# Optimization experiments

Hardware: AMD Instinct MI355X
Metric: run time of the kernel (lower is better)

Reference implementation:

```python
import jax, jax.numpy as jnp
import numpy as np

D_CONV = 4
D_STATE = 16
DT_RANK = 64


def _silu(x):
    return x * jax.nn.sigmoid(x)


def setup_inputs() -> dict:
    key = jax.random.key(0)
    ks = jax.random.split(key, 10)
    B, L, dim = 2, 1024, 1024
    d_inner = 2 * dim
    s = lambda fan: 1.0 / np.sqrt(fan)
    inp = {
        "x": jax.random.normal(ks[0], (B, L, dim), jnp.float32),
        "ln_w": jnp.ones((dim,), jnp.float32),
        "ln_b": jnp.zeros((dim,), jnp.float32),
        "w_in": jax.random.normal(ks[1], (2 * d_inner, dim), jnp.float32) * s(dim),
        "conv_w": jax.random.normal(ks[2], (d_inner, D_CONV), jnp.float32) * s(D_CONV),
        "conv_b": jnp.zeros((d_inner,), jnp.float32),
        "w_xproj": jax.random.normal(ks[3], (DT_RANK + 2 * D_STATE, d_inner), jnp.float32) * s(d_inner),
        "w_dt": jax.random.normal(ks[4], (d_inner, DT_RANK), jnp.float32) * s(DT_RANK),
        "b_dt": jax.random.normal(ks[5], (d_inner,), jnp.float32) * 0.1,
        # S4D-real init: A = -(1..d_state) per channel
        "a_log": jnp.tile(jnp.log(jnp.arange(1, D_STATE + 1, dtype=jnp.float32)), (d_inner, 1)),
        "d_skip": jnp.ones((d_inner,), jnp.float32),
        "w_out": jax.random.normal(ks[6], (dim, d_inner), jnp.float32) * s(d_inner),
    }
    return inp


def reference(x, ln_w, ln_b, w_in, conv_w, conv_b, w_xproj, w_dt, b_dt, a_log, d_skip, w_out):
    B, L, dim = x.shape
    residual = x

    # LayerNorm
    mu = jnp.mean(x, axis=-1, keepdims=True)
    var = jnp.mean((x - mu) ** 2, axis=-1, keepdims=True)
    xn = (x - mu) * jax.lax.rsqrt(var + 1e-5) * ln_w + ln_b

    # in_proj -> (x_ssm, z) each (B, L, d_inner)
    xz = jnp.einsum("bld,ed->ble", xn, w_in)
    d_inner = xz.shape[-1] // 2
    xs, z = xz[..., :d_inner], xz[..., d_inner:]

    # depthwise causal conv1d (kernel D_CONV) + SiLU
    xp = jnp.pad(xs, ((0, 0), (D_CONV - 1, 0), (0, 0)))
    xc = conv_b
    for k in range(D_CONV):
        xc = xc + conv_w[:, k] * xp[:, k : k + L, :]
    u = _silu(xc)  # (B, L, d_inner)

    # x_proj -> dt, B, C
    x_dbl = jnp.einsum("ble,re->blr", u, w_xproj)
    dt_r = x_dbl[..., :DT_RANK]
    B_ssm = x_dbl[..., DT_RANK : DT_RANK + D_STATE]         # (B, L, n)
    C_ssm = x_dbl[..., DT_RANK + D_STATE :]                 # (B, L, n)

    dt = jax.nn.softplus(jnp.einsum("blr,er->ble", dt_r, w_dt) + b_dt)  # (B, L, d_inner)

    A = -jnp.exp(a_log)  # (d_inner, n)
    deltaA = jnp.exp(jnp.einsum("ble,en->blen", dt, A))            # (B, L, e, n)
    deltaBu = jnp.einsum("ble,bln,ble->blen", dt, B_ssm, u)        # (B, L, e, n)

    # selective scan over L
    def step(h, ins):
        dA_t, dBu_t, C_t = ins
        h = dA_t * h + dBu_t                       # (B, e, n)
        y = jnp.einsum("ben,bn->be", h, C_t)
        return h, y

    h0 = jnp.zeros((B, d_inner, D_STATE), xs.dtype)
    _, ys = jax.lax.scan(
        step,
        h0,
        (deltaA.transpose(1, 0, 2, 3), deltaBu.transpose(1, 0, 2, 3), C_ssm.transpose(1, 0, 2)),
    )
    y = ys.transpose(1, 0, 2) + u * d_skip         # (B, L, e)

    y = y * _silu(z)
    out = jnp.einsum("ble,de->bld", y, w_out)
    return residual + out
```

## Files before the change

kernel.cpp:

```cpp
#include <hip/hip_runtime.h>
#include <hip/hip_bf16.h>


#define LC 32
#define NCHUNK 32

typedef short bf16x8 __attribute__((ext_vector_type(8)));
typedef float f32x4  __attribute__((ext_vector_type(4)));

static __device__ __forceinline__ float siluf(float x) { return x / (1.f + __expf(-x)); }
static __device__ __forceinline__ unsigned short f2bf(float f) {
    unsigned int u = __float_as_uint(f);
    unsigned int r = (u + 0x7fffu + ((u >> 16) & 1u)) >> 16;
    return (unsigned short)r;
}
static __device__ __forceinline__ float bfb(unsigned short u) {
    return __uint_as_float(((unsigned int)u) << 16);
}
static __device__ __forceinline__ void gload_lds16(const void* g, void* l) {
    __builtin_amdgcn_global_load_lds(
        (const __attribute__((address_space(1))) void*)g,
        (__attribute__((address_space(3))) void*)l, 16, 0, 0);
}

__global__ __launch_bounds__(256) void setup_kernel(
    const float* __restrict__ w_in,  unsigned short* __restrict__ w_in_b,
    const float* __restrict__ w_out, unsigned short* __restrict__ w_out_b,
    const float* __restrict__ w_dt,  unsigned short* __restrict__ w_dt_b,
    const float* __restrict__ x,
    const float* __restrict__ ln_w,
    const float* __restrict__ ln_b,
    unsigned short* __restrict__ xn)
{
    int bid = blockIdx.x, tid = threadIdx.x;
    if (bid < 6272) {
        int i = bid * 256 + tid;
        const float* in; unsigned short* outp; int j;
        if (i < 1048576)      { in = w_in;  outp = w_in_b;  j = i; }
        else if (i < 1572864) { in = w_out; outp = w_out_b; j = i - 1048576; }
        else if (i < 1605632) { in = w_dt;  outp = w_dt_b;  j = i - 1572864; }
        else return;
        float4 v = reinterpret_cast<const float4*>(in)[j];
        ushort4 o = { f2bf(v.x), f2bf(v.y), f2bf(v.z), f2bf(v.w) };
        reinterpret_cast<ushort4*>(outp)[j] = o;
        return;
    }
    int m = bid - 6272;
    const float4* xr = reinterpret_cast<const float4*>(x) + (size_t)m * 256;
    float4 r = xr[tid];
    float f0 = r.x, f1 = r.y, f2 = r.z, f3 = r.w;
    float s  = f0 + f1 + f2 + f3;
    float s2 = f0*f0 + f1*f1 + f2*f2 + f3*f3;
    #pragma unroll
    for (int off = 32; off > 0; off >>= 1) {
        s  += __shfl_down(s, off);
        s2 += __shfl_down(s2, off);
    }
    __shared__ float red[8];
    if ((tid & 63) == 0) { red[tid >> 6] = s; red[4 + (tid >> 6)] = s2; }
    __syncthreads();
    float st = red[0] + red[1] + red[2] + red[3];
    float qt = red[4] + red[5] + red[6] + red[7];
    float mu   = st * (1.f / 1024.f);
    float var  = qt * (1.f / 1024.f) - mu * mu;
    float rstd = rsqrtf(var + 1e-5f);
    float4 wv = reinterpret_cast<const float4*>(ln_w)[tid];
    float4 bv = reinterpret_cast<const float4*>(ln_b)[tid];
    ushort4 o = { f2bf((f0 - mu) * rstd * wv.x + bv.x),
                  f2bf((f1 - mu) * rstd * wv.y + bv.y),
                  f2bf((f2 - mu) * rstd * wv.z + bv.z),
                  f2bf((f3 - mu) * rstd * wv.w + bv.w) };
    reinterpret_cast<ushort4*>(xn + (size_t)m * 1024)[tid] = o;
}

__global__ __launch_bounds__(256) void gemm_bf16_nt(
    const unsigned short* __restrict__ A, int lda,
    const unsigned short* __restrict__ B, int ldb,
    int Kslice,
    float* __restrict__ C, unsigned short* __restrict__ Cb, int ldc,
    int ep, size_t Cstride)
{
    __shared__ short As[3 * 64 * 32];
    __shared__ short Bs[3 * 128 * 32];
    int tid = threadIdx.x;
    int z = blockIdx.z;
    A += (size_t)z * Kslice;
    B += (size_t)z * Kslice;
    C += (size_t)z * Cstride;

    int gx = gridDim.x;
    int wg = blockIdx.y * gx + blockIdx.x;
    int nwg = gx * gridDim.y;
    int cpx = nwg >> 3;
    int swz = (wg & 7) * cpx + (wg >> 3);
    int bx = swz % gx, by = swz / gx;

    int m0 = by * 64, n0 = bx * 128;
    int lane = tid & 63, wave = tid >> 6;
    int wm = (wave >> 1) * 32, wn = (wave & 1) * 64;
    int frow = lane & 15, fq = lane >> 4;

    f32x4 acc[2][4] = {};

    int lrow = lane >> 2;
    int scol = (lane & 3) * 8;
    const unsigned short* AgL = A + (size_t)(m0 + wave * 16 + lrow) * lda + scol;
    const unsigned short* BgL = B + (size_t)(n0 + wave * 16 + lrow) * ldb + scol;
    int aoff = (wave * 16) * 32;
    int boff = (wave * 16) * 32;

    #pragma unroll
    for (int p = 0; p < 2; ++p) {
        int nk = p * 32;
        gload_lds16(AgL + nk,                    As + p * 2048 + aoff);
        gload_lds16(BgL + nk,                    Bs + p * 4096 + boff);
        gload_lds16(BgL + (size_t)64 * ldb + nk, Bs + p * 4096 + boff + 64 * 32);
    }

    int cur = 0;
    for (int k0 = 0; k0 < Kslice; k0 += 32) {
        if (k0 + 32 < Kslice) {
            asm volatile("s_waitcnt vmcnt(3) lgkmcnt(0)" ::: "memory");
        } else {
            asm volatile("s_waitcnt vmcnt(0) lgkmcnt(0)" ::: "memory");
        }
        __builtin_amdgcn_s_barrier();
        int nk = k0 + 64;
        if (nk < Kslice) {
            int stg = cur - 1; if (stg < 0) stg = 2;
            gload_lds16(AgL + nk,                    As + stg * 2048 + aoff);
            gload_lds16(BgL + nk,                    Bs + stg * 4096 + boff);
            gload_lds16(BgL + (size_t)64 * ldb + nk, Bs + stg * 4096 + boff + 64 * 32);
        }
        const short* Ac = As + cur * 2048;
        const short* Bc = Bs + cur * 4096;
        bf16x8 af[2], bfr[4];
        #pragma unroll
        for (int i = 0; i < 2; ++i)
            af[i] = *reinterpret_cast<const bf16x8*>(Ac + (wm + i * 16 + frow) * 32 + fq * 8);
        #pragma unroll
        for (int j = 0; j < 4; ++j)
            bfr[j] = *reinterpret_cast<const bf16x8*>(Bc + (wn + j * 16 + frow) * 32 + fq * 8);
        #pragma unroll
        for (int i = 0; i < 2; ++i)
            #pragma unroll
            for (int j = 0; j < 4; ++j)
                acc[i][j] = __builtin_amdgcn_mfma_f32_16x16x32_bf16(af[i], bfr[j], acc[i][j], 0, 0, 0);
        cur = (cur == 2) ? 0 : cur + 1;
    }

    int cn = lane & 15, rq = (lane >> 4) * 4;
    #pragma unroll
    for (int i = 0; i < 2; ++i) {
        #pragma unroll
        for (int j = 0; j < 4; ++j) {
            #pragma unroll
            for (int r = 0; r < 4; ++r) {
                int row = m0 + wm + i * 16 + rq + r;
                int col = n0 + wn + j * 16 + cn;
                float v = acc[i][j][r];
                if (ep == 0) {
                    C[(size_t)row * ldc + col] = v;
                } else {
                    Cb[(size_t)row * ldc + col] = f2bf(v);
                }
            }
        }
    }
}

__global__ __launch_bounds__(256) void out_reduce(
    const float* __restrict__ part, const float* __restrict__ x,
    float* __restrict__ out)
{
    int i = blockIdx.x * 256 + threadIdx.x;
    float4 s = reinterpret_cast<const float4*>(x)[i];
    #pragma unroll
    for (int z = 0; z < 4; ++z) {
        float4 p = reinterpret_cast<const float4*>(part + (size_t)z * 2097152)[i];
        s.x += p.x; s.y += p.y; s.z += p.z; s.w += p.w;
    }
    reinterpret_cast<float4*>(out)[i] = s;
}

__global__ __launch_bounds__(256) void xproj_splitk(
    const unsigned short* __restrict__ xz,
    const float* __restrict__ cw,
    const float* __restrict__ cb,
    const float* __restrict__ B,
    unsigned short* __restrict__ u,
    float* __restrict__ part)
{
    __shared__ float As[16][68];
    __shared__ float Bs[16][100];
    int tid = threadIdx.x;
    int m0 = blockIdx.x * 64;
    int k0 = blockIdx.y * 64;
    int tx = tid & 15;
    int ty = tid >> 4;
    float acc[4][6] = {};
    int arow = tid >> 2, akg = (tid & 3) << 2;
    int brow1 = (256 + tid) >> 2, bkg1 = ((256 + tid) & 3) << 2;
    int m = m0 + arow;
    int l = m & 1023;

    for (int ks = 0; ks < 64; ks += 16) {
        int e0 = k0 + ks + akg;
        float xv[4][4];
        #pragma unroll
        for (int kk = 0; kk < 4; ++kk) {
            ushort4 t = make_ushort4(0, 0, 0, 0);
            if (l - 3 + kk >= 0)
                t = *reinterpret_cast<const ushort4*>(xz + (size_t)(m - 3 + kk) * 4096 + e0);
            xv[kk][0] = bfb(t.x); xv[kk][1] = bfb(t.y);
            xv[kk][2] = bfb(t.z); xv[kk][3] = bfb(t.w);
        }
        float4 cbv = *reinterpret_cast<const float4*>(cb + e0);
        float cbs[4] = { cbv.x, cbv.y, cbv.z, cbv.w };
        float res[4];
        #pragma unroll
        for (int j = 0; j < 4; ++j) {
            float4 w = *reinterpret_cast<const float4*>(cw + (size_t)(e0 + j) * 4);
            float a = cbs[j];
            a = fmaf(w.x, xv[0][j], a);
            a = fmaf(w.y, xv[1][j], a);
            a = fmaf(w.z, xv[2][j], a);
            a = fmaf(w.w, xv[3][j], a);
            res[j] = siluf(a);
        }
        ushort4 uo = { f2bf(res[0]), f2bf(res[1]), f2bf(res[2]), f2bf(res[3]) };
        *reinterpret_cast<ushort4*>(u + (size_t)m * 2048 + e0) = uo;

        float4 bv0 = make_float4(0.f, 0.f, 0.f, 0.f), bv1 = bv0;
        if (arow < 96)  bv0 = *reinterpret_cast<const float4*>(B + (size_t)arow * 2048 + k0 + ks + akg);
        if (brow1 < 96) bv1 = *reinterpret_cast<const float4*>(B + (size_t)brow1 * 2048 + k0 + ks + bkg1);
        __syncthreads();
        As[akg + 0][arow] = res[0]; As[akg + 1][arow] = res[1];
        As[akg + 2][arow] = res[2]; As[akg + 3][arow] = res[3];
        if (arow < 96) {
            Bs[akg + 0][arow] = bv0.x; Bs[akg + 1][arow] = bv0.y;
            Bs[akg + 2][arow] = bv0.z; Bs[akg + 3][arow] = bv0.w;
        }
        if (brow1 < 96) {
            Bs[bkg1 + 0][brow1] = bv1.x; Bs[bkg1 + 1][brow1] = bv1.y;
            Bs[bkg1 + 2][brow1] = bv1.z; Bs[bkg1 + 3][brow1] = bv1.w;
        }
        __syncthreads();
        #pragma unroll
        for (int k = 0; k < 16; ++k) {
            float aa[4], bb[6];
            #pragma unroll
            for (int i = 0; i < 4; ++i) aa[i] = As[k][ty * 4 + i];
            #pragma unroll
            for (int j = 0; j < 6; ++j) bb[j] = Bs[k][tx * 6 + j];
            #pragma unroll
            for (int i = 0; i < 4; ++i)
                #pragma unroll
                for (int j = 0; j < 6; ++j)
                    acc[i][j] = fmaf(aa[i], bb[j], acc[i][j]);
        }
    }
    float* p = part + (size_t)blockIdx.y * 196608;
    #pragma unroll
    for (int i = 0; i < 4; ++i)
        #pragma unroll
        for (int j = 0; j < 6; ++j)
            p[(size_t)(m0 + ty * 4 + i) * 96 + tx * 6 + j] = acc[i][j];
}

__global__ __launch_bounds__(256) void xproj_reduce(
    const float* __restrict__ part, float* __restrict__ xdbl)
{
    int i = blockIdx.x * 256 + threadIdx.x;
    float s = 0.f;
    #pragma unroll
    for (int sd = 0; sd < 32; ++sd) s += part[(size_t)sd * 196608 + i];
    xdbl[i] = s;
}

static __device__ __forceinline__ void dt_tile(
    const float* __restrict__ xdbl, const unsigned short* __restrict__ w_dt_b,
    const float* __restrict__ b_dt, size_t rbase, int et,
    int lane, int wave, float dtl[LC][64])
{
    int frow = lane & 15, fq = lane >> 4;
    bf16x8 af[2][2], bfr[2];
    #pragma unroll
    for (int i = 0; i < 2; ++i)
        #pragma unroll
        for (int kk = 0; kk < 2; ++kk) {
            const float* ap = xdbl + (rbase + i * 16 + frow) * 96 + kk * 32 + fq * 8;
            float4 a0 = *reinterpret_cast<const float4*>(ap);
            float4 a1 = *reinterpret_cast<const float4*>(ap + 4);
            bf16x8 t;
            t[0] = (short)f2bf(a0.x); t[1] = (short)f2bf(a0.y);
            t[2] = (short)f2bf(a0.z); t[3] = (short)f2bf(a0.w);
            t[4] = (short)f2bf(a1.x); t[5] = (short)f2bf(a1.y);
            t[6] = (short)f2bf(a1.z); t[7] = (short)f2bf(a1.w);
            af[i][kk] = t;
        }
    #pragma unroll
    for (int kk = 0; kk < 2; ++kk)
        bfr[kk] = *reinterpret_cast<const bf16x8*>(
            w_dt_b + (size_t)(et * 64 + wave * 16 + frow) * 64 + kk * 32 + fq * 8);
    f32x4 dacc[2] = {};
    #pragma unroll
    for (int i = 0; i < 2; ++i)
        #pragma unroll
        for (int kk = 0; kk < 2; ++kk)
            dacc[i] = __builtin_amdgcn_mfma_f32_16x16x32_bf16(af[i][kk], bfr[kk], dacc[i], 0, 0, 0);
    int cn = lane & 15, rq = (lane >> 4) * 4;
    #pragma unroll
    for (int i = 0; i < 2; ++i)
        #pragma unroll
        for (int r = 0; r < 4; ++r) {
            int row = i * 16 + rq + r;
            int col = wave * 16 + cn;
            float v = dacc[i][r] + b_dt[et * 64 + col];
            v = (v > 20.f) ? v : log1pf(__expf(v));
            dtl[row][col] = bfb(f2bf(v));
        }
}

__global__ __launch_bounds__(256) void scan_part1(
    const unsigned short* __restrict__ u,
    const float* __restrict__ xdbl,
    const unsigned short* __restrict__ w_dt_b,
    const float* __restrict__ b_dt,
    const float* __restrict__ a_log,
    float* __restrict__ hpart,
    float* __restrict__ Aprod)
{
    __shared__ float dtl[LC][64];
    int tid = threadIdx.x;
    int ch = tid >> 2, ng = tid & 3;
    int lane = tid & 63, wave = tid >> 6;
    int bid = blockIdx.x;
    int c = bid & 31, et = (bid >> 5) & 31, b = bid >> 10;
    int e = et * 64 + ch;
    size_t rbase = (size_t)b * 1024 + c * LC;

    dt_tile(xdbl, w_dt_b, b_dt, rbase, et, lane, wave, dtl);

    float4 al = *reinterpret_cast<const float4*>(a_log + e * 16 + ng * 4);
    float A0 = -__expf(al.x), A1 = -__expf(al.y), A2 = -__expf(al.z), A3 = -__expf(al.w);
    const unsigned short* u_p  = u  + rbase * 2048 + e;
    const float* b_p  = xdbl + rbase * 96 + 64 + ng * 4;
    float h0 = 0.f, h1 = 0.f, h2 = 0.f, h3 = 0.f;
    float P0 = 1.f, P1 = 1.f, P2 = 1.f, P3 = 1.f;
    float u_c  = bfb(u_p[0]);
    float4 B_c = *reinterpret_cast<const float4*>(b_p);
    __syncthreads();
    #pragma unroll 8
    for (int l = 0; l < LC; ++l) {
        float u_n  = bfb(u_p[(size_t)(l + 1) * 2048]);
        float4 B_n = *reinterpret_cast<const float4*>(b_p + (size_t)(l + 1) * 96);
        float dtv = dtl[l][ch];
        float du = dtv * u_c;
        float d0 = __expf(dtv * A0), d1 = __expf(dtv * A1);
        float d2 = __expf(dtv * A2), d3 = __expf(dtv * A3);
        h0 = fmaf(d0, h0, du * B_c.x); P0 *= d0;
        h1 = fmaf(d1, h1, du * B_c.y); P1 *= d1;
        h2 = fmaf(d2, h2, du * B_c.z); P2 *= d2;
        h3 = fmaf(d3, h3, du * B_c.w); P3 *= d3;
        u_c = u_n; B_c = B_n;
    }
    size_t oidx = (size_t)c * 65536 + ((size_t)b * 2048 + e) * 16 + ng * 4;
    *reinterpret_cast<float4*>(hpart + oidx) = make_float4(h0, h1, h2, h3);
    *reinterpret_cast<float4*>(Aprod + oidx) = make_float4(P0, P1, P2, P3);
}

__global__ __launch_bounds__(256) void scan_combine(
    const float* __restrict__ hpart,
    const float* __restrict__ Aprod,
    float* __restrict__ hinit)
{
    int t = blockIdx.x * 256 + threadIdx.x;
    float h = 0.f;
    #pragma unroll 8
    for (int c = 0; c < NCHUNK; ++c) {
        hinit[(size_t)c * 65536 + t] = h;
        float P  = Aprod[(size_t)c * 65536 + t];
        float hp = hpart[(size_t)c * 65536 + t];
        h = fmaf(P, h, hp);
    }
}

__global__ __launch_bounds__(256) void scan_part2(
    const unsigned short* __restrict__ u,
    const float* __restrict__ xdbl,
    const unsigned short* __restrict__ w_dt_b,
    const float* __restrict__ b_dt,
    const unsigned short* __restrict__ xz,
    const float* __restrict__ a_log,
    const float* __restrict__ d_skip,
    const float* __restrict__ hinit,
    unsigned short* __restrict__ y)
{
    __shared__ float dtl[LC][64];
    int tid = threadIdx.x;
    int ch = tid >> 2, ng = tid & 3;
    int lane = tid & 63, wave = tid >> 6;
    int bid = blockIdx.x;
    int c = bid & 31, et = (bid >> 5) & 31, b = bid >> 10;
    int e = et * 64 + ch;
    size_t rbase = (size_t)b * 1024 + c * LC;

    dt_tile(xdbl, w_dt_b, b_dt, rbase, et, lane, wave, dtl);

    float4 al = *reinterpret_cast<const float4*>(a_log + e * 16 + ng * 4);
    float A0 = -__expf(al.x), A1 = -__expf(al.y), A2 = -__expf(al.z), A3 = -__expf(al.w);
    float dsk = d_skip[e];
    const unsigned short* u_p  = u  + rbase * 2048 + e;
    const unsigned short* z_p  = xz + rbase * 4096 + 2048 + e;
    const float* bc_p = xdbl + rbase * 96 + 64 + ng * 4;
    unsigned short* y_p = y + rbase * 2048 + e;
    size_t oidx = (size_t)c * 65536 + ((size_t)b * 2048 + e) * 16 + ng * 4;
    float4 hi = *reinterpret_cast<const float4*>(hinit + oidx);
    float h0 = hi.x, h1 = hi.y, h2 = hi.z, h3 = hi.w;
    float u_c  = bfb(u_p[0]);
    float4 B_c = *reinterpret_cast<const float4*>(bc_p);
    float4 C_c = *reinterpret_cast<const float4*>(bc_p + 16);
    __syncthreads();
    #pragma unroll 8
    for (int l = 0; l < LC; ++l) {
        float u_n  = bfb(u_p[(size_t)(l + 1) * 2048]);
        float4 B_n = *reinterpret_cast<const float4*>(bc_p + (size_t)(l + 1) * 96);
        float4 C_n = *reinterpret_cast<const float4*>(bc_p + (size_t)(l + 1) * 96 + 16);
        float dtv = dtl[l][ch];
        float du = dtv * u_c;
        float d0 = __expf(dtv * A0), d1 = __expf(dtv * A1);
        float d2 = __expf(dtv * A2), d3 = __expf(dtv * A3);
        h0 = fmaf(d0, h0, du * B_c.x);
        h1 = fmaf(d1, h1, du * B_c.y);
        h2 = fmaf(d2, h2, du * B_c.z);
        h3 = fmaf(d3, h3, du * B_c.w);
        float p = h0 * C_c.x + h1 * C_c.y + h2 * C_c.z + h3 * C_c.w;
        p += __shfl_xor(p, 1);
        p += __shfl_xor(p, 2);
        if (ng == 0) {
            float zv = bfb(z_p[(size_t)l * 4096]);
            y_p[(size_t)l * 2048] = f2bf((p + u_c * dsk) * siluf(zv));
        }
        u_c = u_n; B_c = B_n; C_c = C_n;
    }
}

extern "C" void kernel_launch(void* const* d_in, const int* in_sizes, int n_in,
                              void* d_out, int out_size, void* d_ws, size_t ws_size,
                              hipStream_t stream) {
    const float* x       = (const float*)d_in[0];
    const float* ln_w    = (const float*)d_in[1];
    const float* ln_b    = (const float*)d_in[2];
    const float* w_in    = (const float*)d_in[3];
    const float* conv_w  = (const float*)d_in[4];
    const float* conv_b  = (const float*)d_in[5];
    const float* w_xproj = (const float*)d_in[6];
    const float* w_dt    = (const float*)d_in[7];
    const float* b_dt    = (const float*)d_in[8];
    const float* a_log   = (const float*)d_in[9];
    const float* d_skip  = (const float*)d_in[10];
    const float* w_out   = (const float*)d_in[11];
    float* out = (float*)d_out;

    float* ws = (float*)d_ws;
    unsigned short* xn_b    = (unsigned short*)(ws);
    unsigned short* xz_b    = (unsigned short*)(ws + 1048576);
    unsigned short* u_b     = (unsigned short*)(ws + 5242880);
    float* xdbl  = ws + 7340032;
    float* hpart = ws + 9633792;
    float* Aprod = ws + 13828096;
    float* hinit = ws + 18022400;
    unsigned short* y_b     = (unsigned short*)(ws + 22216704);
    unsigned short* w_in_b  = (unsigned short*)(ws + 24313856);
    unsigned short* w_out_b = (unsigned short*)(ws + 26411008);
    unsigned short* w_dt_b  = (unsigned short*)(ws + 27459584);
    float* xpart = ws + 9633792;
    float* opart = ws + 1048576;

    setup_kernel<<<8320, 256, 0, stream>>>(w_in, w_in_b, w_out, w_out_b, w_dt, w_dt_b,
                                           x, ln_w, ln_b, xn_b);
    gemm_bf16_nt<<<dim3(32, 32, 1), 256, 0, stream>>>(xn_b, 1024, w_in_b, 1024, 1024,
                                                      nullptr, xz_b, 4096, 3, 0);
    xproj_splitk<<<dim3(32, 32), 256, 0, stream>>>(xz_b, conv_w, conv_b, w_xproj,
                                                   u_b, xpart);
    xproj_reduce<<<768, 256, 0, stream>>>(xpart, xdbl);
    scan_part1<<<2048, 256, 0, stream>>>(u_b, xdbl, w_dt_b, b_dt, a_log, hpart, Aprod);
    scan_combine<<<256, 256, 0, stream>>>(hpart, Aprod, hinit);
    scan_part2<<<2048, 256, 0, stream>>>(u_b, xdbl, w_dt_b, b_dt, xz_b, a_log,
                                         d_skip, hinit, y_b);
    gemm_bf16_nt<<<dim3(8, 32, 4), 256, 0, stream>>>(y_b, 2048, w_out_b, 2048, 512,
                                                     opart, nullptr, 1024, 0, 2097152);
    out_reduce<<<2048, 256, 0, stream>>>(opart, x, out);
}
```

Measured before the change: 264.7 us.

## Map one thread per channel with all 16 states in scan kernels

The chunked selective-scan kernels are remapped so each thread owns one channel and keeps all 16 state values in registers. Previously four threads shared a channel with four states each, and the output needed a cross-lane shuffle reduction. Blocks now cover 256 channels, and chunk length drops from 32 to 16, giving 64 chunks. The dt tile computation is widened to 256 channels per block. This removes the shuffles and redundant u/z loads, and makes the u/z/y accesses coalesced across channels. The cost is higher register pressure, a longer serial scan_combine over 64 chunks, and twice the hpart/Aprod/hinit traffic.

Measured after the change: 278.1 us. +5.1%, slower.

```diff
diff --git a/kernel.cpp b/kernel.cpp
--- a/kernel.cpp
+++ b/kernel.cpp
@@ -2,8 +2,8 @@
 #include <hip/hip_bf16.h>
 
 
-#define LC 32
-#define NCHUNK 32
+#define LC 16
+#define NCHUNK 64
 
 typedef short bf16x8 __attribute__((ext_vector_type(8)));
 typedef float f32x4  __attribute__((ext_vector_type(4)));
@@ -278,47 +278,45 @@
     xdbl[i] = s;
 }
 
-static __device__ __forceinline__ void dt_tile(
+static __device__ __forceinline__ void dt_tile256(
     const float* __restrict__ xdbl, const unsigned short* __restrict__ w_dt_b,
     const float* __restrict__ b_dt, size_t rbase, int et,
-    int lane, int wave, float dtl[LC][64])
+    int lane, int wave, float dtl[LC][256])
 {
     int frow = lane & 15, fq = lane >> 4;
-    bf16x8 af[2][2], bfr[2];
-    #pragma unroll
-    for (int i = 0; i < 2; ++i)
+    bf16x8 af[2];
+    #pragma unroll
+    for (int kk = 0; kk < 2; ++kk) {
+        const float* ap = xdbl + (rbase + frow) * 96 + kk * 32 + fq * 8;
+        float4 a0 = *reinterpret_cast<const float4*>(ap);
+        float4 a1 = *reinterpret_cast<const float4*>(ap + 4);
+        bf16x8 t;
+        t[0] = (short)f2bf(a0.x); t[1] = (short)f2bf(a0.y);
+        t[2] = (short)f2bf(a0.z); t[3] = (short)f2bf(a0.w);
+        t[4] = (short)f2bf(a1.x); t[5] = (short)f2bf(a1.y);
+        t[6] = (short)f2bf(a1.z); t[7] = (short)f2bf(a1.w);
+        af[kk] = t;
+    }
+    f32x4 dacc[4] = {};
+    #pragma unroll
+    for (int j = 0; j < 4; ++j)
         #pragma unroll
         for (int kk = 0; kk < 2; ++kk) {
-            const float* ap = xdbl + (rbase + i * 16 + frow) * 96 + kk * 32 + fq * 8;
-            float4 a0 = *reinterpret_cast<const float4*>(ap);
-            float4 a1 = *reinterpret_cast<const float4*>(ap + 4);
-            bf16x8 t;
-            t[0] = (short)f2bf(a0.x); t[1] = (short)f2bf(a0.y);
-            t[2] = (short)f2bf(a0.z); t[3] = (short)f2bf(a0.w);
-            t[4] = (short)f2bf(a1.x); t[5] = (short)f2bf(a1.y);
-            t[6] = (short)f2bf(a1.z); t[7] = (short)f2bf(a1.w);
-            af[i][kk] = t;
-        }
-    #pragma unroll
-    for (int kk = 0; kk < 2; ++kk)
-        bfr[kk] = *reinterpret_cast<const bf16x8*>(
-            w_dt_b + (size_t)(et * 64 + wave * 16 + frow) * 64 + kk * 32 + fq * 8);
-    f32x4 dacc[2] = {};
-    #pragma unroll
-    for (int i = 0; i < 2; ++i)
-        #pragma unroll
-        for (int kk = 0; kk < 2; ++kk)
-            dacc[i] = __builtin_amdgcn_mfma_f32_16x16x32_bf16(af[i][kk], bfr[kk], dacc[i], 0, 0, 0);
+            int row_e = et * 256 + wave * 64 + j * 16 + frow;
+            bf16x8 bfr = *reinterpret_cast<const bf16x8*>(
+                w_dt_b + (size_t)row_e * 64 + kk * 32 + fq * 8);
+            dacc[j] = __builtin_amdgcn_mfma_f32_16x16x32_bf16(af[kk], bfr, dacc[j], 0, 0, 0);
+        }
     int cn = lane & 15, rq = (lane >> 4) * 4;
     #pragma unroll
-    for (int i = 0; i < 2; ++i)
+    for (int j = 0; j < 4; ++j)
         #pragma unroll
         for (int r = 0; r < 4; ++r) {
-            int row = i * 16 + rq + r;
-            int col = wave * 16 + cn;
-            float v = dacc[i][r] + b_dt[et * 64 + col];
+            int lrow = rq + r;
+            int ecol = wave * 64 + j * 16 + cn;
+            float v = dacc[j][r] + b_dt[et * 256 + ecol];
             v = (v > 20.f) ? v : log1pf(__expf(v));
-            dtl[row][col] = bfb(f2bf(v));
+            dtl[lrow][ecol] = bfb(f2bf(v));
         }
 }
 
@@ -331,43 +329,57 @@
     float* __restrict__ hpart,
     float* __restrict__ Aprod)
 {
-    __shared__ float dtl[LC][64];
+    __shared__ float dtl[LC][256];
     int tid = threadIdx.x;
-    int ch = tid >> 2, ng = tid & 3;
     int lane = tid & 63, wave = tid >> 6;
     int bid = blockIdx.x;
-    int c = bid & 31, et = (bid >> 5) & 31, b = bid >> 10;
-    int e = et * 64 + ch;
+    int c = bid & 63, et = (bid >> 6) & 7, b = bid >> 9;
+    int e = et * 256 + tid;
     size_t rbase = (size_t)b * 1024 + c * LC;
 
-    dt_tile(xdbl, w_dt_b, b_dt, rbase, et, lane, wave, dtl);
-
-    float4 al = *reinterpret_cast<const float4*>(a_log + e * 16 + ng * 4);
-    float A0 = -__expf(al.x), A1 = -__expf(al.y), A2 = -__expf(al.z), A3 = -__expf(al.w);
-    const unsigned short* u_p  = u  + rbase * 2048 + e;
-    const float* b_p  = xdbl + rbase * 96 + 64 + ng * 4;
-    float h0 = 0.f, h1 = 0.f, h2 = 0.f, h3 = 0.f;
-    float P0 = 1.f, P1 = 1.f, P2 = 1.f, P3 = 1.f;
-    float u_c  = bfb(u_p[0]);
-    float4 B_c = *reinterpret_cast<const float4*>(b_p);
+    dt_tile256(xdbl, w_dt_b, b_dt, rbase, et, lane, wave, dtl);
+
+    float A[16];
+    #pragma unroll
+    for (int q = 0; q < 4; ++q) {
+        float4 al = *reinterpret_cast<const float4*>(a_log + (size_t)e * 16 + q * 4);
+        A[q * 4 + 0] = -__expf(al.x); A[q * 4 + 1] = -__expf(al.y);
+        A[q * 4 + 2] = -__expf(al.z); A[q * 4 + 3] = -__expf(al.w);
+    }
+    float h[16], P[16];
+    #pragma unroll
+    for (int n = 0; n < 16; ++n) { h[n] = 0.f; P[n] = 1.f; }
+
+    const unsigned short* u_p = u + rbase * 2048 + e;
+    const float* b_p = xdbl + rbase * 96 + 64;
     __syncthreads();
-    #pragma unroll 8
+    #pragma unroll
     for (int l = 0; l < LC; ++l) {
-        float u_n  = bfb(u_p[(size_t)(l + 1) * 2048]);
-        float4 B_n = *reinterpret_cast<const float4*>(b_p + (size_t)(l + 1) * 96);
-        float dtv = dtl[l][ch];
+        float dtv = dtl[l][tid];
+        float u_c = bfb(u_p[(size_t)l * 2048]);
+        float Bv[16];
+        #pragma unroll
+        for (int q = 0; q < 4; ++q) {
+            float4 bv = *reinterpret_cast<const float4*>(b_p + (size_t)l * 96 + q * 4);
+            Bv[q * 4 + 0] = bv.x; Bv[q * 4 + 1] = bv.y;
+            Bv[q * 4 + 2] = bv.z; Bv[q * 4 + 3] = bv.w;
+        }
         float du = dtv * u_c;
-        float d0 = __expf(dtv * A0), d1 = __expf(dtv * A1);
-        float d2 = __expf(dtv * A2), d3 = __expf(dtv * A3);
-        h0 = fmaf(d0, h0, du * B_c.x); P0 *= d0;
-        h1 = fmaf(d1, h1, du * B_c.y); P1 *= d1;
-        h2 = fmaf(d2, h2, du * B_c.z); P2 *= d2;
-        h3 = fmaf(d3, h3, du * B_c.w); P3 *= d3;
-        u_c = u_n; B_c = B_n;
-    }
-    size_t oidx = (size_t)c * 65536 + ((size_t)b * 2048 + e) * 16 + ng * 4;
-    *reinterpret_cast<float4*>(hpart + oidx) = make_float4(h0, h1, h2, h3);
-    *reinterpret_cast<float4*>(Aprod + oidx) = make_float4(P0, P1, P2, P3);
+        #pragma unroll
+        for (int n = 0; n < 16; ++n) {
+            float d = __expf(dtv * A[n]);
+            h[n] = fmaf(d, h[n], du * Bv[n]);
+            P[n] *= d;
+        }
+    }
+    size_t oidx = (size_t)c * 65536 + ((size_t)b * 2048 + e) * 16;
+    #pragma unroll
+    for (int q = 0; q < 4; ++q) {
+        *reinterpret_cast<float4*>(hpart + oidx + q * 4) =
+            make_float4(h[q * 4], h[q * 4 + 1], h[q * 4 + 2], h[q * 4 + 3]);
+        *reinterpret_cast<float4*>(Aprod + oidx + q * 4) =
+            make_float4(P[q * 4], P[q * 4 + 1], P[q * 4 + 2], P[q * 4 + 3]);
+    }
 }
 
 __global__ __launch_bounds__(256) void scan_combine(
@@ -397,52 +409,62 @@
     const float* __restrict__ hinit,
     unsigned short* __restrict__ y)
 {
-    __shared__ float dtl[LC][64];
+    __shared__ float dtl[LC][256];
     int tid = threadIdx.x;
-    int ch = tid >> 2, ng = tid & 3;
     int lane = tid & 63, wave = tid >> 6;
     int bid = blockIdx.x;
-    int c = bid & 31, et = (bid >> 5) & 31, b = bid >> 10;
-    int e = et * 64 + ch;
+    int c = bid & 63, et = (bid >> 6) & 7, b = bid >> 9;
+    int e = et * 256 + tid;
     size_t rbase = (size_t)b * 1024 + c * LC;
 
-    dt_tile(xdbl, w_dt_b, b_dt, rbase, et, lane, wave, dtl);
-
-    float4 al = *reinterpret_cast<const float4*>(a_log + e * 16 + ng * 4);
-    float A0 = -__expf(al.x), A1 = -__expf(al.y), A2 = -__expf(al.z), A3 = -__expf(al.w);
+    dt_tile256(xdbl, w_dt_b, b_dt, rbase, et, lane, wave, dtl);
+
+    float A[16];
+    #pragma unroll
+    for (int q = 0; q < 4; ++q) {
+        float4 al = *reinterpret_cast<const float4*>(a_log + (size_t)e * 16 + q * 4);
+        A[q * 4 + 0] = -__expf(al.x); A[q * 4 + 1] = -__expf(al.y);
+        A[q * 4 + 2] = -__expf(al.z); A[q * 4 + 3] = -__expf(al.w);
+    }
     float dsk = d_skip[e];
-    const unsigned short* u_p  = u  + rbase * 2048 + e;
-    const unsigned short* z_p  = xz + rbase * 4096 + 2048 + e;
-    const float* bc_p = xdbl + rbase * 96 + 64 + ng * 4;
+    float h[16];
+    size_t oidx = (size_t)c * 65536 + ((size_t)b * 2048 + e) * 16;
+    #pragma unroll
+    for (int q = 0; q < 4; ++q) {
+        float4 hq = *reinterpret_cast<const float4*>(hinit + oidx + q * 4);
+        h[q * 4 + 0] = hq.x; h[q * 4 + 1] = hq.y;
+        h[q * 4 + 2] = hq.z; h[q * 4 + 3] = hq.w;
+    }
+
+    const unsigned short* u_p = u + rbase * 2048 + e;
+    const unsigned short* z_p = xz + rbase * 4096 + 2048 + e;
+    const float* b_p = xdbl + rbase * 96 + 64;
     unsigned short* y_p = y + rbase * 2048 + e;
-    size_t oidx = (size_t)c * 65536 + ((size_t)b * 2048 + e) * 16 + ng * 4;
-    float4 hi = *reinterpret_cast<const float4*>(hinit + oidx);
-    float h0 = hi.x, h1 = hi.y, h2 = hi.z, h3 = hi.w;
-    float u_c  = bfb(u_p[0]);
-    float4 B_c = *reinterpret_cast<const float4*>(bc_p);
-    float4 C_c = *reinterpret_cast<const float4*>(bc_p + 16);
     __syncthreads();
-    #pragma unroll 8
+    #pragma unroll
     for (int l = 0; l < LC; ++l) {
-        float u_n  = bfb(u_p[(size_t)(l + 1) * 2048]);
-        float4 B_n = *reinterpret_cast<const float4*>(bc_p + (size_t)(l + 1) * 96);
-        float4 C_n = *reinterpret_cast<const float4*>(bc_p + (size_t)(l + 1) * 96 + 16);
-        float dtv = dtl[l][ch];
+        float dtv = dtl[l][tid];
+        float u_c = bfb(u_p[(size_t)l * 2048]);
+        float Bv[16], Cv[16];
+        #pragma unroll
+        for (int q = 0; q < 4; ++q) {
+            float4 bv = *reinterpret_cast<const float4*>(b_p + (size_t)l * 96 + q * 4);
+            float4 cv = *reinterpret_cast<const float4*>(b_p + (size_t)l * 96 + 16 + q * 4);
+            Bv[q * 4 + 0] = bv.x; Bv[q * 4 + 1] = bv.y;
+            Bv[q * 4 + 2] = bv.z; Bv[q * 4 + 3] = bv.w;
+            Cv[q * 4 + 0] = cv.x; Cv[q * 4 + 1] = cv.y;
+            Cv[q * 4 + 2] = cv.z; Cv[q * 4 + 3] = cv.w;
+        }
         float du = dtv * u_c;
-        float d0 = __expf(dtv * A0), d1 = __expf(dtv * A1);
-        float d2 = __expf(dtv * A2), d3 = __expf(dtv * A3);
-        h0 = fmaf(d0, h0, du * B_c.x);
-        h1 = fmaf(d1, h1, du * B_c.y);
-        h2 = fmaf(d2, h2, du * B_c.z);
-        h3 = fmaf(d3, h3, du * B_c.w);
-        float p = h0 * C_c.x + h1 * C_c.y + h2 * C_c.z + h3 * C_c.w;
-        p += __shfl_xor(p, 1);
-        p += __shfl_xor(p, 2);
-        if (ng == 0) {
-            float zv = bfb(z_p[(size_t)l * 4096]);
-            y_p[(size_t)l * 2048] = f2bf((p + u_c * dsk) * siluf(zv));
-        }
-        u_c = u_n; B_c = B_n; C_c = C_n;
+        float p = 0.f;
+        #pragma unroll
+        for (int n = 0; n < 16; ++n) {
+            float d = __expf(dtv * A[n]);
+            h[n] = fmaf(d, h[n], du * Bv[n]);
+            p = fmaf(h[n], Cv[n], p);
+        }
+        float zv = bfb(z_p[(size_t)l * 4096]);
+        y_p[(size_t)l * 2048] = f2bf((p + u_c * dsk) * siluf(zv));
     }
 }
 
@@ -485,9 +507,9 @@
     xproj_splitk<<<dim3(32, 32), 256, 0, stream>>>(xz_b, conv_w, conv_b, w_xproj,
                                                    u_b, xpart);
     xproj_reduce<<<768, 256, 0, stream>>>(xpart, xdbl);
-    scan_part1<<<2048, 256, 0, stream>>>(u_b, xdbl, w_dt_b, b_dt, a_log, hpart, Aprod);
+    scan_part1<<<1024, 256, 0, stream>>>(u_b, xdbl, w_dt_b, b_dt, a_log, hpart, Aprod);
     scan_combine<<<256, 256, 0, stream>>>(hpart, Aprod, hinit);
-    scan_part2<<<2048, 256, 0, stream>>>(u_b, xdbl, w_dt_b, b_dt, xz_b, a_log,
+    scan_part2<<<1024, 256, 0, stream>>>(u_b, xdbl, w_dt_b, b_dt, xz_b, a_log,
                                          d_skip, hinit, y_b);
     gemm_bf16_nt<<<dim3(8, 32, 4), 256, 0, stream>>>(y_b, 2048, w_out_b, 2048, 512,
                                                      opart, nullptr, 1024, 0, 2097152);
```
